# Performance work log

Measured on AMD Instinct MI355X. Metric: run time of the kernel, lower is better.

## Reference

```python
import jax, jax.numpy as jnp
import numpy as np


def setup_inputs() -> dict:
    key = jax.random.key(0)
    k1, k2, k3 = jax.random.split(key, 3)
    N = 20000
    # valid [x1, y1, x2, y2] boxes: centers in [0,1000), sizes in [1,101)
    xy = jax.random.uniform(k1, (N, 2), dtype=jnp.float32) * 1000.0
    wh = jax.random.uniform(k2, (N, 2), dtype=jnp.float32) * 100.0 + 1.0
    boxes = jnp.concatenate([xy, xy + wh], axis=1)
    scores = jax.random.uniform(k3, (N,), dtype=jnp.float32)
    return {
        "boxes": boxes,
        "scores": scores,
        "max_output_size": 1000,
        "iou_threshold": 0.5,
        "scores_threshold": 0.1,
    }


def reference(boxes, scores, max_output_size, iou_threshold, scores_threshold):
    boxes = boxes.astype(jnp.float32)
    scores = scores.astype(jnp.float32)
    N = boxes.shape[0]

    # score filtering: instead of physically filtering (dynamic shape),
    # mark below-threshold boxes as pre-suppressed and push them to the
    # end of the stable descending sort with -inf keys.
    valid = scores > scores_threshold
    sort_key = jnp.where(valid, scores, -jnp.inf)
    order = jnp.argsort(-sort_key)  # jnp.argsort is stable -> stable descending

    sboxes = boxes[order]                      # [N,4] score-sorted boxes
    svalid = valid[order]
    sorig = order.astype(jnp.int32)            # original indices, sorted
    areas = (sboxes[:, 2] - sboxes[:, 0]) * (sboxes[:, 3] - sboxes[:, 1])
    idx = jnp.arange(N)

    def body(carry, i):
        suppressed, selected, count = carry
        can = jnp.logical_and(~suppressed[i], count < max_output_size)
        selected = jnp.where(can, selected.at[count].set(sorig[i]), selected)
        # vectorized IoU of box i against all boxes (only j > i matter)
        b = sboxes[i]
        x1 = jnp.maximum(b[0], sboxes[:, 0])
        y1 = jnp.maximum(b[1], sboxes[:, 1])
        x2 = jnp.minimum(b[2], sboxes[:, 2])
        y2 = jnp.minimum(b[3], sboxes[:, 3])
        inter = jnp.maximum(x2 - x1, 0.0) * jnp.maximum(y2 - y1, 0.0)
        union = jnp.maximum(areas[i] + areas - inter, 1e-6)
        iou = inter / union
        suppressed = suppressed | (can & (idx > i) & (iou >= iou_threshold))
        count = count + can.astype(jnp.int32)
        return (suppressed, selected, count), None

    init = (~svalid, jnp.zeros(max_output_size, dtype=jnp.int32), jnp.int32(0))
    (_, selected, count), _ = jax.lax.scan(body, init, idx)
    return selected, count
```

## Files before the change

kernel.cpp:

```cpp
#include <hip/hip_runtime.h>
#include <cstdint>

typedef unsigned long long u64;

#define TOPK 2048
#define MW2 (TOPK / 64)
#define CAND 4096
#define HIST_BLOCKS 8
#define COMPACT_BLOCKS 32
#define FB_WORDS 1024


__device__ __forceinline__ unsigned score_ud(float s, float thr) {
    unsigned u = __float_as_uint(s);
    u ^= (u >> 31) ? 0xFFFFFFFFu : 0x80000000u;
    unsigned ud = ~u;
    if (!(s > thr)) ud = 0xFFFFFFFFu;
    return ud;
}

__global__ __launch_bounds__(256) void hist_kernel(const float* __restrict__ scores,
                                                   const float* __restrict__ thrPtr,
                                                   int* __restrict__ slices,
                                                   int* __restrict__ meta, int N) {
    __shared__ int h[4096];
    int tid = threadIdx.x;
    for (int b = tid; b < 4096; b += 256) h[b] = 0;
    if (blockIdx.x == 0 && tid == 0) meta[0] = 0;
    __syncthreads();
    float thr = *thrPtr;
    for (int i = blockIdx.x * 256 + tid; i < N; i += HIST_BLOCKS * 256) {
        unsigned ud = score_ud(scores[i], thr);
        if (ud != 0xFFFFFFFFu) atomicAdd(&h[ud >> 20], 1);
    }
    __syncthreads();
    int* myslice = slices + blockIdx.x * 4096;
    for (int b = tid; b < 4096; b += 256) myslice[b] = h[b];
}

__global__ __launch_bounds__(256) void compact_kernel(
        const float* __restrict__ scores, const float* __restrict__ thrPtr,
        const int* __restrict__ slices, int* __restrict__ meta,
        u64* __restrict__ ckeys, int N, int maxNeed) {
    __shared__ int bins[4096];
    __shared__ int shC;
    int tid = threadIdx.x, lane = tid & 63;
    {
        const int4* sl = (const int4*)slices;
        int4* bo = (int4*)bins;
#pragma unroll
        for (int k = 0; k < 4; ++k) {
            int p = k * 256 + tid;
            int4 a = sl[p];
            int4 v1 = sl[1024 + p];
            int4 v2 = sl[2 * 1024 + p];
            int4 v3 = sl[3 * 1024 + p];
            int4 v4 = sl[4 * 1024 + p];
            int4 v5 = sl[5 * 1024 + p];
            int4 v6 = sl[6 * 1024 + p];
            int4 v7 = sl[7 * 1024 + p];
            a.x += v1.x + v2.x + v3.x + v4.x + v5.x + v6.x + v7.x;
            a.y += v1.y + v2.y + v3.y + v4.y + v5.y + v6.y + v7.y;
            a.z += v1.z + v2.z + v3.z + v4.z + v5.z + v6.z + v7.z;
            a.w += v1.w + v2.w + v3.w + v4.w + v5.w + v6.w + v7.w;
            bo[p] = a;
        }
    }
    __syncthreads();
    if (tid < 64) {
        int base = lane * 64;
        int sum = 0;
        for (int b = 0; b < 64; ++b) sum += bins[base + ((b + lane) & 63)];
        int incl = sum;
        for (int off = 1; off < 64; off <<= 1) {
            int o = __shfl_up(incl, off, 64);
            if (lane >= off) incl += o;
        }
        int total = __shfl(incl, 63, 64);
        int need = (maxNeed < total) ? maxNeed : total;
        u64 ok = __ballot(incl >= need);
        int L = (ok != 0ull) ? (int)__builtin_ctzll(ok) : 0;
        if (lane == L) {
            int acc = incl - sum;
            int C = base, Msel = acc;
            for (int b = 0; b < 64; ++b) {
                acc += bins[base + b];
                if (acc >= need) { C = base + b; Msel = acc; break; }
            }
            if (need <= 0) { C = -1; Msel = 0; }
            shC = C;
            if (blockIdx.x == 0) {
                meta[2] = Msel;
                meta[3] = (Msel > CAND) ? 1 : 0;
            }
        }
        if (lane == 0 && blockIdx.x == 0) meta[1] = total;
    }
    __syncthreads();
    int C = shC;
    float thr = *thrPtr;
    for (int i0 = blockIdx.x * 256; i0 < N; i0 += COMPACT_BLOCKS * 256) {
        int i = i0 + tid;
        bool sel = false;
        unsigned ud = 0;
        if (i < N) {
            ud = score_ud(scores[i], thr);
            sel = (ud != 0xFFFFFFFFu) && ((int)(ud >> 20) <= C);
        }
        u64 ball = __ballot(sel);
        if (ball) {
            int cntw = __popcll(ball);
            int base = 0;
            if (lane == 0) base = atomicAdd(&meta[0], cntw);
            base = __shfl(base, 0, 64);
            if (sel) {
                int slot = base + __popcll(ball & ((1ull << lane) - 1ull));
                if (slot < CAND) ckeys[slot] = ((u64)ud << 32) | (unsigned)i;
            }
        }
    }
}

template<int K>
__device__ __forceinline__ void wave_chain(u64 (&r)[4], int wave, int lane) {
    if (K >= 256) {
#pragma unroll
        for (int e = 0; e < 2; ++e) {
            bool up = ((((wave << 8) | (e << 6) | lane) & K) == 0);
            if ((r[e] > r[e + 2]) == up) { u64 tmp = r[e]; r[e] = r[e + 2]; r[e + 2] = tmp; }
        }
    }
    if (K >= 128) {
#pragma unroll
        for (int e = 0; e < 4; e += 2) {
            bool up = ((((wave << 8) | (e << 6) | lane) & K) == 0);
            if ((r[e] > r[e + 1]) == up) { u64 tmp = r[e]; r[e] = r[e + 1]; r[e + 1] = tmp; }
        }
    }
#pragma unroll
    for (int j = 32; j >= 1; j >>= 1) {
        if (2 * j <= K) {
#pragma unroll
            for (int e = 0; e < 4; ++e) {
                bool up = ((((wave << 8) | (e << 6) | lane) & K) == 0);
                u64 o = __shfl_xor(r[e], j, 64);
                bool lower = ((lane & j) == 0);
                bool keepMin = (up == lower);
                u64 mn = (r[e] < o) ? r[e] : o;
                u64 mx = (r[e] < o) ? o : r[e];
                r[e] = keepMin ? mn : mx;
            }
        }
    }
}

__global__ __launch_bounds__(1024) void sort_gather_kernel(
        const u64* __restrict__ ckeys, const int* __restrict__ meta,
        const float* __restrict__ boxes,
        float* __restrict__ sx1, float* __restrict__ sy1,
        float* __restrict__ sx2, float* __restrict__ sy2,
        float* __restrict__ areas, int* __restrict__ sorig,
        u64* __restrict__ validw) {
    __shared__ u64 lk[CAND];
    int tid = threadIdx.x, lane = tid & 63, wave = tid >> 6;
    int M = meta[2];
    if (M > CAND) M = CAND;
    u64 r[4];
#pragma unroll
    for (int e = 0; e < 4; ++e) {
        int s = (wave << 8) + (e << 6) + lane;
        r[e] = (s < M) ? ckeys[s] : ~0ull;
    }
    wave_chain<2>(r, wave, lane);
    wave_chain<4>(r, wave, lane);
    wave_chain<8>(r, wave, lane);
    wave_chain<16>(r, wave, lane);
    wave_chain<32>(r, wave, lane);
    wave_chain<64>(r, wave, lane);
    wave_chain<128>(r, wave, lane);
    wave_chain<256>(r, wave, lane);
#pragma unroll
    for (int lvl = 0; lvl < 4; ++lvl) {
        const int K = 512 << lvl;
#pragma unroll
        for (int e = 0; e < 4; ++e) lk[(wave << 8) + (e << 6) + lane] = r[e];
        __syncthreads();
        for (int j = K / 2; j >= 256; j >>= 1) {
            for (int p = tid; p < CAND / 2; p += 1024) {
                int i = ((p & ~(j - 1)) << 1) | (p & (j - 1));
                int l = i + j;
                bool up = ((i & K) == 0);
                u64 a = lk[i], b = lk[l];
                if ((a > b) == up) { lk[i] = b; lk[l] = a; }
            }
            __syncthreads();
        }
#pragma unroll
        for (int e = 0; e < 4; ++e) r[e] = lk[(wave << 8) + (e << 6) + lane];
        switch (lvl) {
            case 0: wave_chain<512>(r, wave, lane); break;
            case 1: wave_chain<1024>(r, wave, lane); break;
            case 2: wave_chain<2048>(r, wave, lane); break;
            default: wave_chain<4096>(r, wave, lane); break;
        }
    }
    if (wave < (TOPK / 256)) {
#pragma unroll
        for (int e = 0; e < 4; ++e) {
            int s = (wave << 8) + (e << 6) + lane;
            u64 k = r[e];
            unsigned hi = (unsigned)(k >> 32), lo = (unsigned)k;
            bool valid = (hi != 0xFFFFFFFFu);
            u64 ball = __ballot(valid);
            if (lane == 0) validw[s >> 6] = ball;
            float4 b; b.x = 0.f; b.y = 0.f; b.z = 0.f; b.w = 0.f;
            if (valid) b = ((const float4*)boxes)[lo];
            sx1[s] = b.x; sy1[s] = b.y; sx2[s] = b.z; sy2[s] = b.w;
            areas[s] = (b.z - b.x) * (b.w - b.y);
            sorig[s] = valid ? (int)lo : 0;
        }
    }
}

__global__ __launch_bounds__(64) void mask2_kernel(
        const float* __restrict__ sx1, const float* __restrict__ sy1,
        const float* __restrict__ sx2, const float* __restrict__ sy2,
        const float* __restrict__ areas, const float* __restrict__ iouThrPtr,
        u64* __restrict__ maskT, u64* __restrict__ diagT) {
    int wi = blockIdx.x, wj = blockIdx.y;
    if (wj < wi) return;
    __shared__ float jx1[64], jy1[64], jx2[64], jy2[64], ja[64];
    __shared__ u64 rowLDS[64];
    int t = threadIdx.x;
    int j0 = wj << 6;
    jx1[t] = sx1[j0 + t]; jy1[t] = sy1[j0 + t];
    jx2[t] = sx2[j0 + t]; jy2[t] = sy2[j0 + t];
    ja[t] = areas[j0 + t];
    __syncthreads();
    int i = (wi << 6) + t;
    float thr = *iouThrPtr;
    float ix1 = sx1[i], iy1 = sy1[i], ix2 = sx2[i], iy2 = sy2[i], ia = areas[i];
    u64 bits = 0;
    for (int jj = 0; jj < 64; ++jj) {
        int j = j0 + jj;
        if (j > i) {
            float xx1 = fmaxf(ix1, jx1[jj]);
            float yy1 = fmaxf(iy1, jy1[jj]);
            float xx2 = fminf(ix2, jx2[jj]);
            float yy2 = fminf(iy2, jy2[jj]);
            float ww = fmaxf(xx2 - xx1, 0.0f);
            float hh = fmaxf(yy2 - yy1, 0.0f);
            float inter = ww * hh;
            float uni = fmaxf(ia + ja[jj] - inter, 1e-6f);
            if (inter / uni >= thr) bits |= 1ull << jj;
        }
    }
    rowLDS[t] = bits;
    __syncthreads();
    u64 col = 0;
    for (int r = 0; r < 64; ++r) col |= ((rowLDS[r] >> t) & 1ull) << r;
    maskT[(size_t)(j0 + t) * MW2 + wi] = col;
    if (wi == wj) diagT[(wi << 6) + t] = col;
}

__global__ __launch_bounds__(1024) void scan2_kernel(
        const u64* __restrict__ maskT, const u64* __restrict__ diagT,
        const u64* __restrict__ validw, const int* __restrict__ sorig,
        const int* __restrict__ meta,
        const float* __restrict__ boxes, const float* __restrict__ scores,
        const float* __restrict__ iouThrPtr, const float* __restrict__ scoreThrPtr,
        int* __restrict__ out, int N, int maxOut) {
    __shared__ u64 diagLDS[TOPK];
    __shared__ u64 selw[MW2];
    __shared__ u64 validwLDS[MW2];
    __shared__ u64 ballots[4];
    __shared__ int selLDS[TOPK];
    __shared__ int cntSh;
    __shared__ int validScanSh;
    __shared__ u64 aliveW[FB_WORDS];
    __shared__ u64 keyRed[16];
    __shared__ u64 winKeySh;
    int tid = threadIdx.x, lane = tid & 63, wave = tid >> 6;

    for (int k = tid; k < TOPK; k += 1024) diagLDS[k] = diagT[k];
    if (tid < MW2) { selw[tid] = 0ull; validwLDS[tid] = validw[tid]; }
    if (tid == 0) { cntSh = 0; validScanSh = 0; }

    ulonglong2 a0, a1, a2, a3;
    int cc = tid >> 2, g = tid & 3;
    if (tid < 256) {
        const ulonglong2* p = (const ulonglong2*)(maskT + (size_t)cc * MW2 + g * 8);
        a0 = p[0]; a1 = p[1]; a2 = p[2]; a3 = p[3];
    }
    __syncthreads();

    int cnt = 0;
    for (int w = 0; w < MW2; ++w) {
        if (tid < 256) {
            u64 wd0 = a0.x, wd1 = a0.y, wd2 = a1.x, wd3 = a1.y;
            u64 wd4 = a2.x, wd5 = a2.y, wd6 = a3.x, wd7 = a3.y;
            int wr0 = g * 8;
            u64 acc = 0;
            if (wr0 + 0 < w) acc |= wd0 & selw[wr0 + 0];
            if (wr0 + 1 < w) acc |= wd1 & selw[wr0 + 1];
            if (wr0 + 2 < w) acc |= wd2 & selw[wr0 + 2];
            if (wr0 + 3 < w) acc |= wd3 & selw[wr0 + 3];
            if (wr0 + 4 < w) acc |= wd4 & selw[wr0 + 4];
            if (wr0 + 5 < w) acc |= wd5 & selw[wr0 + 5];
            if (wr0 + 6 < w) acc |= wd6 & selw[wr0 + 6];
            if (wr0 + 7 < w) acc |= wd7 & selw[wr0 + 7];
            acc |= __shfl_xor(acc, 1, 64);
            acc |= __shfl_xor(acc, 2, 64);
            u64 B = __ballot(acc != 0ull);
            if (lane == 0) ballots[wave] = B;
            if (w + 1 < MW2) {
                const ulonglong2* p = (const ulonglong2*)(maskT + (size_t)((w + 1) * 64 + cc) * MW2 + g * 8);
                a0 = p[0]; a1 = p[1]; a2 = p[2]; a3 = p[3];
            }
        }
        __syncthreads();
        if (wave == 0) {
            u64 bv = ballots[lane >> 4];
            bool crossk = (bv >> ((lane & 15) << 2)) & 1ull;
            bool alv = ((validwLDS[w] >> lane) & 1ull) && !crossk;
            u64 inm = diagLDS[(w << 6) | lane];
            u64 sel = __ballot(alv);
            for (int it = 0; it < 64; ++it) {
                bool killed = (inm & sel) != 0ull;
                u64 ns = __ballot(alv && !killed);
                if (ns == sel) break;
                sel = ns;
            }
            int room = maxOut - cnt;
            int tot = __popcll(sel);
            u64 below = (1ull << lane) - 1ull;
            if (tot > room) {
                bool keep = ((sel >> lane) & 1ull) && (__popcll(sel & below) < room);
                sel = __ballot(keep);
                tot = room;
            }
            if ((sel >> lane) & 1ull) {
                int pos = cnt + __popcll(sel & below);
                selLDS[pos] = (w << 6) | lane;
            }
            if (lane == 0) { selw[w] = sel; cntSh = cnt + tot; }
        }
        __syncthreads();
        cnt = cntSh;
        if (cnt >= maxOut) break;
    }

    if (tid < MW2) atomicAdd(&validScanSh, __popcll(validwLDS[tid]));
    __syncthreads();
    int vt = meta[1];
    int f2 = meta[3];
    bool complete = (f2 == 0) && ((cnt >= maxOut) || (validScanSh >= vt));
    if (complete) {
        for (int k = tid; k < cnt; k += 1024) out[k] = sorig[selLDS[k]];
        for (int k = cnt + tid; k < maxOut; k += 1024) out[k] = 0;
        if (tid == 0) out[maxOut] = cnt;
        return;
    }

    float sThr = *scoreThrPtr, iThr = *iouThrPtr;
    for (int e0 = wave << 6; e0 < N; e0 += 1024) {
        int e = e0 + lane;
        bool a = (e < N) && (scores[e] > sThr);
        u64 ball = __ballot(a);
        if (lane == 0) aliveW[e0 >> 6] = ball;
    }
    __syncthreads();
    int fcnt = 0;
    while (fcnt < maxOut) {
        u64 best = 0;
        for (int e = tid; e < N; e += 1024) {
            if ((aliveW[e >> 6] >> (e & 63)) & 1ull) {
                float s = scores[e];
                unsigned u = __float_as_uint(s);
                u ^= (u >> 31) ? 0xFFFFFFFFu : 0x80000000u;
                u64 k = ((u64)u << 32) | (unsigned)(~e);
                if (k > best) best = k;
            }
        }
#pragma unroll
        for (int off = 32; off >= 1; off >>= 1) {
            u64 o = __shfl_xor(best, off, 64);
            if (o > best) best = o;
        }
        if (lane == 0) keyRed[wave] = best;
        __syncthreads();
        if (tid == 0) {
            u64 b = 0;
            for (int p = 0; p < 16; ++p) if (keyRed[p] > b) b = keyRed[p];
            winKeySh = b;
        }
        __syncthreads();
        u64 wk = winKeySh;
        if (wk == 0ull) break;
        int win = (int)(~(unsigned)wk);
        if (tid == 0) out[fcnt] = win;
        ++fcnt;
        float4 wb = ((const float4*)boxes)[win];
        float wa = (wb.z - wb.x) * (wb.w - wb.y);
        for (int e0 = wave << 6; e0 < N; e0 += 1024) {
            int e = e0 + lane;
            bool kill = false;
            if (e < N && ((aliveW[e0 >> 6] >> lane) & 1ull)) {
                if (e == win) kill = true;
                else {
                    float4 bb = ((const float4*)boxes)[e];
                    float xx1 = fmaxf(wb.x, bb.x), yy1 = fmaxf(wb.y, bb.y);
                    float xx2 = fminf(wb.z, bb.z), yy2 = fminf(wb.w, bb.w);
                    float inter = fmaxf(xx2 - xx1, 0.0f) * fmaxf(yy2 - yy1, 0.0f);
                    float ba = (bb.z - bb.x) * (bb.w - bb.y);
                    float uni = fmaxf(wa + ba - inter, 1e-6f);
                    kill = (inter / uni >= iThr);
                }
            }
            u64 kb = __ballot(kill);
            if (lane == 0 && kb) aliveW[e0 >> 6] &= ~kb;
        }
        __syncthreads();
    }
    for (int k = fcnt + tid; k < maxOut; k += 1024) out[k] = 0;
    if (tid == 0) out[maxOut] = fcnt;
}

extern "C" void kernel_launch(void* const* d_in, const int* in_sizes, int n_in,
                              void* d_out, int out_size, void* d_ws, size_t ws_size,
                              hipStream_t stream) {
    const float* boxes       = (const float*)d_in[0];
    const float* scores      = (const float*)d_in[1];
    const float* iouThrPtr   = (const float*)d_in[3];
    const float* scoreThrPtr = (const float*)d_in[4];

    int N = in_sizes[0] / 4;
    int maxOut = out_size - 1;

    char* ws = (char*)d_ws;
    size_t off = 0;
    auto take = [&](size_t b) { void* p = ws + off; off = (off + b + 255) & ~(size_t)255; return p; };
    int*   slices = (int*)  take((size_t)HIST_BLOCKS * 4096 * 4);
    int*   meta   = (int*)  take(256);
    u64*   ckeys  = (u64*)  take((size_t)CAND * 8);
    float* sx1    = (float*)take(TOPK * 4);
    float* sy1    = (float*)take(TOPK * 4);
    float* sx2    = (float*)take(TOPK * 4);
    float* sy2    = (float*)take(TOPK * 4);
    float* areas  = (float*)take(TOPK * 4);
    int*   sorig  = (int*)  take(TOPK * 4);
    u64*   validw = (u64*)  take(MW2 * 8);
    u64*   maskT  = (u64*)  take((size_t)TOPK * MW2 * 8);
    u64*   diagT  = (u64*)  take((size_t)MW2 * 64 * 8);
    (void)ws_size;

    hist_kernel<<<HIST_BLOCKS, 256, 0, stream>>>(scores, scoreThrPtr, slices, meta, N);
    compact_kernel<<<COMPACT_BLOCKS, 256, 0, stream>>>(scores, scoreThrPtr, slices, meta,
                                                       ckeys, N, TOPK);
    sort_gather_kernel<<<1, 1024, 0, stream>>>(ckeys, meta, boxes, sx1, sy1, sx2, sy2,
                                               areas, sorig, validw);
    mask2_kernel<<<dim3(MW2, MW2), 64, 0, stream>>>(sx1, sy1, sx2, sy2, areas, iouThrPtr,
                                                    maskT, diagT);
    scan2_kernel<<<1, 1024, 0, stream>>>(maskT, diagT, validw, sorig, meta,
                                         boxes, scores, iouThrPtr, scoreThrPtr,
                                         (int*)d_out, N, maxOut);
}
```

Baseline: 76.75 us.

## Fuse histogram, compaction and sort into a single-block select kernel

Merges the multi-block histogram, compaction and bitonic sort kernels into one 1024-thread block that builds the score histogram in shared memory, compacts candidates directly into shared memory, and sorts them in place. This removes two kernel launches and the global round-trips through slices and ckeys, plus global atomics. In exchange, the scan over 20000 scores runs twice on a single CU instead of being spread across many blocks.

```diff
diff --git a/kernel.cpp b/kernel.cpp
--- a/kernel.cpp
+++ b/kernel.cpp
@@ -6,8 +6,6 @@
 #define TOPK 2048
 #define MW2 (TOPK / 64)
 #define CAND 4096
-#define HIST_BLOCKS 8
-#define COMPACT_BLOCKS 32
 #define FB_WORDS 1024
 
 
@@ -19,51 +17,63 @@
     return ud;
 }
 
-__global__ __launch_bounds__(256) void hist_kernel(const float* __restrict__ scores,
-                                                   const float* __restrict__ thrPtr,
-                                                   int* __restrict__ slices,
-                                                   int* __restrict__ meta, int N) {
-    __shared__ int h[4096];
-    int tid = threadIdx.x;
-    for (int b = tid; b < 4096; b += 256) h[b] = 0;
-    if (blockIdx.x == 0 && tid == 0) meta[0] = 0;
-    __syncthreads();
+template<int K>
+__device__ __forceinline__ void wave_chain(u64 (&r)[4], int wave, int lane) {
+    if (K >= 256) {
+#pragma unroll
+        for (int e = 0; e < 2; ++e) {
+            bool up = ((((wave << 8) | (e << 6) | lane) & K) == 0);
+            if ((r[e] > r[e + 2]) == up) { u64 tmp = r[e]; r[e] = r[e + 2]; r[e + 2] = tmp; }
+        }
+    }
+    if (K >= 128) {
+#pragma unroll
+        for (int e = 0; e < 4; e += 2) {
+            bool up = ((((wave << 8) | (e << 6) | lane) & K) == 0);
+            if ((r[e] > r[e + 1]) == up) { u64 tmp = r[e]; r[e] = r[e + 1]; r[e + 1] = tmp; }
+        }
+    }
+#pragma unroll
+    for (int j = 32; j >= 1; j >>= 1) {
+        if (2 * j <= K) {
+#pragma unroll
+            for (int e = 0; e < 4; ++e) {
+                bool up = ((((wave << 8) | (e << 6) | lane) & K) == 0);
+                u64 o = __shfl_xor(r[e], j, 64);
+                bool lower = ((lane & j) == 0);
+                bool keepMin = (up == lower);
+                u64 mn = (r[e] < o) ? r[e] : o;
+                u64 mx = (r[e] < o) ? o : r[e];
+                r[e] = keepMin ? mn : mx;
+            }
+        }
+    }
+}
+
+__global__ __launch_bounds__(1024) void fused_select_kernel(
+        const float* __restrict__ scores, const float* __restrict__ thrPtr,
+        const float* __restrict__ boxes, int* __restrict__ meta,
+        float* __restrict__ sx1, float* __restrict__ sy1,
+        float* __restrict__ sx2, float* __restrict__ sy2,
+        float* __restrict__ areas, int* __restrict__ sorig,
+        u64* __restrict__ validw, int N, int maxNeed) {
+    __shared__ int bins[4096];
+    __shared__ u64 lk[CAND];
+    __shared__ int shC;
+    __shared__ int shTicket;
+    int tid = threadIdx.x, lane = tid & 63, wave = tid >> 6;
+
+    for (int b = tid; b < 4096; b += 1024) bins[b] = 0;
+    for (int u = tid; u < CAND; u += 1024) lk[u] = ~0ull;
+    if (tid == 0) shTicket = 0;
+    __syncthreads();
+
     float thr = *thrPtr;
-    for (int i = blockIdx.x * 256 + tid; i < N; i += HIST_BLOCKS * 256) {
-        unsigned ud = score_ud(scores[i], thr);
-        if (ud != 0xFFFFFFFFu) atomicAdd(&h[ud >> 20], 1);
-    }
-    __syncthreads();
-    int* myslice = slices + blockIdx.x * 4096;
-    for (int b = tid; b < 4096; b += 256) myslice[b] = h[b];
-}
-
-__global__ __launch_bounds__(256) void compact_kernel(
-        const float* __restrict__ scores, const float* __restrict__ thrPtr,
-        const int* __restrict__ slices, int* __restrict__ meta,
-        u64* __restrict__ ckeys, int N, int maxNeed) {
-    __shared__ int bins[4096];
-    __shared__ int shC;
-    int tid = threadIdx.x, lane = tid & 63;
-    {
-        const int4* sl = (const int4*)slices;
-        int4* bo = (int4*)bins;
-#pragma unroll
-        for (int k = 0; k < 4; ++k) {
-            int p = k * 256 + tid;
-            int4 a = sl[p];
-            int4 v1 = sl[1024 + p];
-            int4 v2 = sl[2 * 1024 + p];
-            int4 v3 = sl[3 * 1024 + p];
-            int4 v4 = sl[4 * 1024 + p];
-            int4 v5 = sl[5 * 1024 + p];
-            int4 v6 = sl[6 * 1024 + p];
-            int4 v7 = sl[7 * 1024 + p];
-            a.x += v1.x + v2.x + v3.x + v4.x + v5.x + v6.x + v7.x;
-            a.y += v1.y + v2.y + v3.y + v4.y + v5.y + v6.y + v7.y;
-            a.z += v1.z + v2.z + v3.z + v4.z + v5.z + v6.z + v7.z;
-            a.w += v1.w + v2.w + v3.w + v4.w + v5.w + v6.w + v7.w;
-            bo[p] = a;
+    for (int i0 = 0; i0 < N; i0 += 1024) {
+        int i = i0 + tid;
+        if (i < N) {
+            unsigned ud = score_ud(scores[i], thr);
+            if (ud != 0xFFFFFFFFu) atomicAdd(&bins[ud >> 20], 1);
         }
     }
     __syncthreads();
@@ -89,17 +99,14 @@
             }
             if (need <= 0) { C = -1; Msel = 0; }
             shC = C;
-            if (blockIdx.x == 0) {
-                meta[2] = Msel;
-                meta[3] = (Msel > CAND) ? 1 : 0;
-            }
-        }
-        if (lane == 0 && blockIdx.x == 0) meta[1] = total;
+            meta[2] = Msel;
+            meta[3] = (Msel > CAND) ? 1 : 0;
+        }
+        if (lane == 0) meta[1] = total;
     }
     __syncthreads();
     int C = shC;
-    float thr = *thrPtr;
-    for (int i0 = blockIdx.x * 256; i0 < N; i0 += COMPACT_BLOCKS * 256) {
+    for (int i0 = 0; i0 < N; i0 += 1024) {
         int i = i0 + tid;
         bool sel = false;
         unsigned ud = 0;
@@ -111,66 +118,18 @@
         if (ball) {
             int cntw = __popcll(ball);
             int base = 0;
-            if (lane == 0) base = atomicAdd(&meta[0], cntw);
+            if (lane == 0) base = atomicAdd(&shTicket, cntw);
             base = __shfl(base, 0, 64);
             if (sel) {
                 int slot = base + __popcll(ball & ((1ull << lane) - 1ull));
-                if (slot < CAND) ckeys[slot] = ((u64)ud << 32) | (unsigned)i;
-            }
-        }
-    }
-}
-
-template<int K>
-__device__ __forceinline__ void wave_chain(u64 (&r)[4], int wave, int lane) {
-    if (K >= 256) {
-#pragma unroll
-        for (int e = 0; e < 2; ++e) {
-            bool up = ((((wave << 8) | (e << 6) | lane) & K) == 0);
-            if ((r[e] > r[e + 2]) == up) { u64 tmp = r[e]; r[e] = r[e + 2]; r[e + 2] = tmp; }
-        }
-    }
-    if (K >= 128) {
-#pragma unroll
-        for (int e = 0; e < 4; e += 2) {
-            bool up = ((((wave << 8) | (e << 6) | lane) & K) == 0);
-            if ((r[e] > r[e + 1]) == up) { u64 tmp = r[e]; r[e] = r[e + 1]; r[e + 1] = tmp; }
-        }
-    }
-#pragma unroll
-    for (int j = 32; j >= 1; j >>= 1) {
-        if (2 * j <= K) {
-#pragma unroll
-            for (int e = 0; e < 4; ++e) {
-                bool up = ((((wave << 8) | (e << 6) | lane) & K) == 0);
-                u64 o = __shfl_xor(r[e], j, 64);
-                bool lower = ((lane & j) == 0);
-                bool keepMin = (up == lower);
-                u64 mn = (r[e] < o) ? r[e] : o;
-                u64 mx = (r[e] < o) ? o : r[e];
-                r[e] = keepMin ? mn : mx;
-            }
-        }
-    }
-}
-
-__global__ __launch_bounds__(1024) void sort_gather_kernel(
-        const u64* __restrict__ ckeys, const int* __restrict__ meta,
-        const float* __restrict__ boxes,
-        float* __restrict__ sx1, float* __restrict__ sy1,
-        float* __restrict__ sx2, float* __restrict__ sy2,
-        float* __restrict__ areas, int* __restrict__ sorig,
-        u64* __restrict__ validw) {
-    __shared__ u64 lk[CAND];
-    int tid = threadIdx.x, lane = tid & 63, wave = tid >> 6;
-    int M = meta[2];
-    if (M > CAND) M = CAND;
+                if (slot < CAND) lk[slot] = ((u64)ud << 32) | (unsigned)i;
+            }
+        }
+    }
+    __syncthreads();
     u64 r[4];
 #pragma unroll
-    for (int e = 0; e < 4; ++e) {
-        int s = (wave << 8) + (e << 6) + lane;
-        r[e] = (s < M) ? ckeys[s] : ~0ull;
-    }
+    for (int e = 0; e < 4; ++e) r[e] = lk[(wave << 8) + (e << 6) + lane];
     wave_chain<2>(r, wave, lane);
     wave_chain<4>(r, wave, lane);
     wave_chain<8>(r, wave, lane);
@@ -440,9 +399,7 @@
     char* ws = (char*)d_ws;
     size_t off = 0;
     auto take = [&](size_t b) { void* p = ws + off; off = (off + b + 255) & ~(size_t)255; return p; };
-    int*   slices = (int*)  take((size_t)HIST_BLOCKS * 4096 * 4);
     int*   meta   = (int*)  take(256);
-    u64*   ckeys  = (u64*)  take((size_t)CAND * 8);
     float* sx1    = (float*)take(TOPK * 4);
     float* sy1    = (float*)take(TOPK * 4);
     float* sx2    = (float*)take(TOPK * 4);
@@ -454,11 +411,9 @@
     u64*   diagT  = (u64*)  take((size_t)MW2 * 64 * 8);
     (void)ws_size;
 
-    hist_kernel<<<HIST_BLOCKS, 256, 0, stream>>>(scores, scoreThrPtr, slices, meta, N);
-    compact_kernel<<<COMPACT_BLOCKS, 256, 0, stream>>>(scores, scoreThrPtr, slices, meta,
-                                                       ckeys, N, TOPK);
-    sort_gather_kernel<<<1, 1024, 0, stream>>>(ckeys, meta, boxes, sx1, sy1, sx2, sy2,
-                                               areas, sorig, validw);
+    fused_select_kernel<<<1, 1024, 0, stream>>>(scores, scoreThrPtr, boxes, meta,
+                                                sx1, sy1, sx2, sy2, areas, sorig,
+                                                validw, N, TOPK);
     mask2_kernel<<<dim3(MW2, MW2), 64, 0, stream>>>(sx1, sy1, sx2, sy2, areas, iouThrPtr,
                                                     maskT, diagT);
     scan2_kernel<<<1, 1024, 0, stream>>>(maskT, diagT, validw, sorig, meta,
```

Result: faster. 75.21 us (-2.0%).

## Run greedy NMS block scan in a single wave with double-buffered mask columns

Applied to the files above, without the earlier changes.

The serial 64-box block scan now runs entirely in wave 0. Each lane loads its full 32-word suppression column into registers and double-buffers the next column, which removes the two block-wide barriers per step and the cross-wave ballot exchange. The histogram stage also doubles its block count, and the compaction sums the slices in a loop. The trade-off is higher register pressure, since 64 ulonglong2 values are held per lane, and all cross-block AND work now falls on one wave instead of four.

```diff
diff --git a/kernel.cpp b/kernel.cpp
--- a/kernel.cpp
+++ b/kernel.cpp
@@ -6,7 +6,7 @@
 #define TOPK 2048
 #define MW2 (TOPK / 64)
 #define CAND 4096
-#define HIST_BLOCKS 8
+#define HIST_BLOCKS 16
 #define COMPACT_BLOCKS 32
 #define FB_WORDS 1024
 
@@ -51,19 +51,14 @@
 #pragma unroll
         for (int k = 0; k < 4; ++k) {
             int p = k * 256 + tid;
-            int4 a = sl[p];
-            int4 v1 = sl[1024 + p];
-            int4 v2 = sl[2 * 1024 + p];
-            int4 v3 = sl[3 * 1024 + p];
-            int4 v4 = sl[4 * 1024 + p];
-            int4 v5 = sl[5 * 1024 + p];
-            int4 v6 = sl[6 * 1024 + p];
-            int4 v7 = sl[7 * 1024 + p];
-            a.x += v1.x + v2.x + v3.x + v4.x + v5.x + v6.x + v7.x;
-            a.y += v1.y + v2.y + v3.y + v4.y + v5.y + v6.y + v7.y;
-            a.z += v1.z + v2.z + v3.z + v4.z + v5.z + v6.z + v7.z;
-            a.w += v1.w + v2.w + v3.w + v4.w + v5.w + v6.w + v7.w;
-            bo[p] = a;
+            int ax = 0, ay = 0, az = 0, aw = 0;
+#pragma unroll
+            for (int s = 0; s < HIST_BLOCKS; ++s) {
+                int4 v = sl[s * 1024 + p];
+                ax += v.x; ay += v.y; az += v.z; aw += v.w;
+            }
+            int4 o; o.x = ax; o.y = ay; o.z = az; o.w = aw;
+            bo[p] = o;
         }
     }
     __syncthreads();
@@ -273,7 +268,6 @@
     __shared__ u64 diagLDS[TOPK];
     __shared__ u64 selw[MW2];
     __shared__ u64 validwLDS[MW2];
-    __shared__ u64 ballots[4];
     __shared__ int selLDS[TOPK];
     __shared__ int cntSh;
     __shared__ int validScanSh;
@@ -285,73 +279,68 @@
     for (int k = tid; k < TOPK; k += 1024) diagLDS[k] = diagT[k];
     if (tid < MW2) { selw[tid] = 0ull; validwLDS[tid] = validw[tid]; }
     if (tid == 0) { cntSh = 0; validScanSh = 0; }
-
-    ulonglong2 a0, a1, a2, a3;
-    int cc = tid >> 2, g = tid & 3;
-    if (tid < 256) {
-        const ulonglong2* p = (const ulonglong2*)(maskT + (size_t)cc * MW2 + g * 8);
-        a0 = p[0]; a1 = p[1]; a2 = p[2]; a3 = p[3];
-    }
-    __syncthreads();
-
-    int cnt = 0;
-    for (int w = 0; w < MW2; ++w) {
-        if (tid < 256) {
-            u64 wd0 = a0.x, wd1 = a0.y, wd2 = a1.x, wd3 = a1.y;
-            u64 wd4 = a2.x, wd5 = a2.y, wd6 = a3.x, wd7 = a3.y;
-            int wr0 = g * 8;
-            u64 acc = 0;
-            if (wr0 + 0 < w) acc |= wd0 & selw[wr0 + 0];
-            if (wr0 + 1 < w) acc |= wd1 & selw[wr0 + 1];
-            if (wr0 + 2 < w) acc |= wd2 & selw[wr0 + 2];
-            if (wr0 + 3 < w) acc |= wd3 & selw[wr0 + 3];
-            if (wr0 + 4 < w) acc |= wd4 & selw[wr0 + 4];
-            if (wr0 + 5 < w) acc |= wd5 & selw[wr0 + 5];
-            if (wr0 + 6 < w) acc |= wd6 & selw[wr0 + 6];
-            if (wr0 + 7 < w) acc |= wd7 & selw[wr0 + 7];
-            acc |= __shfl_xor(acc, 1, 64);
-            acc |= __shfl_xor(acc, 2, 64);
-            u64 B = __ballot(acc != 0ull);
-            if (lane == 0) ballots[wave] = B;
-            if (w + 1 < MW2) {
-                const ulonglong2* p = (const ulonglong2*)(maskT + (size_t)((w + 1) * 64 + cc) * MW2 + g * 8);
-                a0 = p[0]; a1 = p[1]; a2 = p[2]; a3 = p[3];
-            }
-        }
-        __syncthreads();
-        if (wave == 0) {
-            u64 bv = ballots[lane >> 4];
-            bool crossk = (bv >> ((lane & 15) << 2)) & 1ull;
-            bool alv = ((validwLDS[w] >> lane) & 1ull) && !crossk;
-            u64 inm = diagLDS[(w << 6) | lane];
-            u64 sel = __ballot(alv);
-            for (int it = 0; it < 64; ++it) {
-                bool killed = (inm & sel) != 0ull;
-                u64 ns = __ballot(alv && !killed);
-                if (ns == sel) break;
-                sel = ns;
-            }
-            int room = maxOut - cnt;
-            int tot = __popcll(sel);
-            u64 below = (1ull << lane) - 1ull;
-            if (tot > room) {
-                bool keep = ((sel >> lane) & 1ull) && (__popcll(sel & below) < room);
-                sel = __ballot(keep);
-                tot = room;
-            }
-            if ((sel >> lane) & 1ull) {
-                int pos = cnt + __popcll(sel & below);
-                selLDS[pos] = (w << 6) | lane;
-            }
-            if (lane == 0) { selw[w] = sel; cntSh = cnt + tot; }
-        }
-        __syncthreads();
-        cnt = cntSh;
-        if (cnt >= maxOut) break;
-    }
+    __syncthreads();
+
+    if (wave == 0) {
+        ulonglong2 A[16], B[16];
+#define LOADCOL(BUF, W)                                                          \
+        {                                                                        \
+            const ulonglong2* p =                                                \
+                (const ulonglong2*)(maskT + (size_t)(((W) << 6) | lane) * MW2);  \
+            _Pragma("unroll")                                                    \
+            for (int k = 0; k < 16; ++k) BUF[k] = p[k];                          \
+        }
+#define PROCESS(BUF, W)                                                          \
+        {                                                                        \
+            u64 kill = 0;                                                        \
+            _Pragma("unroll")                                                    \
+            for (int k = 0; k < 16; ++k)                                         \
+                kill |= (BUF[k].x & selw[2 * k]) | (BUF[k].y & selw[2 * k + 1]); \
+            bool alv = ((validwLDS[W] >> lane) & 1ull) && (kill == 0ull);        \
+            u64 inm = diagLDS[((W) << 6) | lane];                                \
+            u64 sel = __ballot(alv);                                             \
+            for (int it = 0; it < 64; ++it) {                                    \
+                bool killed = (inm & sel) != 0ull;                               \
+                u64 ns = __ballot(alv && !killed);                               \
+                if (ns == sel) break;                                            \
+                sel = ns;                                                        \
+            }                                                                    \
+            int room = maxOut - cnt;                                             \
+            int tot = __popcll(sel);                                             \
+            u64 below = (1ull << lane) - 1ull;                                   \
+            if (tot > room) {                                                    \
+                bool keep = ((sel >> lane) & 1ull) &&                            \
+                            (__popcll(sel & below) < room);                      \
+                sel = __ballot(keep);                                            \
+                tot = room;                                                      \
+            }                                                                    \
+            if ((sel >> lane) & 1ull) {                                          \
+                int pos = cnt + __popcll(sel & below);                           \
+                selLDS[pos] = ((W) << 6) | lane;                                 \
+            }                                                                    \
+            if (lane == 0) selw[W] = sel;                                        \
+            cnt += tot;                                                          \
+            done = (cnt >= maxOut);                                              \
+        }
+        int cnt = 0;
+        bool done = false;
+        LOADCOL(A, 0);
+        for (int w = 0; w < MW2 && !done; w += 2) {
+            if (w + 1 < MW2) LOADCOL(B, w + 1);
+            PROCESS(A, w);
+            if (done || w + 1 >= MW2) break;
+            if (w + 2 < MW2) LOADCOL(A, w + 2);
+            PROCESS(B, w + 1);
+        }
+#undef LOADCOL
+#undef PROCESS
+        if (lane == 0) cntSh = cnt;
+    }
+    __syncthreads();
 
     if (tid < MW2) atomicAdd(&validScanSh, __popcll(validwLDS[tid]));
     __syncthreads();
+    int cnt = cntSh;
     int vt = meta[1];
     int f2 = meta[3];
     bool complete = (f2 == 0) && ((cnt >= maxOut) || (validScanSh >= vt));
```

New measurement: 93.06 us. 1.21x slower.

## Replace single-block bitonic sort with multi-block rank-by-counting gather

Applied to the files above, without the earlier changes.

The 4096-element bitonic sort, which ran in one 1024-thread block, is replaced by a rank kernel launched over 64 blocks. Each block loads all candidate keys into LDS and computes each key's rank by counting smaller keys, then scatters the box and original index directly to that rank. Boxes are now stored as float4, and mask2 recomputes areas on the fly. The valid-word bitmask is derived from the candidate count instead of being stored. This trades O(M^2) comparisons and redundant LDS loads per block for parallelism across many CUs instead of one, and it relies on keys being unique, which the embedded index guarantees.

```diff
diff --git a/kernel.cpp b/kernel.cpp
--- a/kernel.cpp
+++ b/kernel.cpp
@@ -8,6 +8,7 @@
 #define CAND 4096
 #define HIST_BLOCKS 8
 #define COMPACT_BLOCKS 32
+#define RANK_BLOCKS (CAND / 64)
 #define FB_WORDS 1024
 
 
@@ -121,111 +122,40 @@
     }
 }
 
-template<int K>
-__device__ __forceinline__ void wave_chain(u64 (&r)[4], int wave, int lane) {
-    if (K >= 256) {
-#pragma unroll
-        for (int e = 0; e < 2; ++e) {
-            bool up = ((((wave << 8) | (e << 6) | lane) & K) == 0);
-            if ((r[e] > r[e + 2]) == up) { u64 tmp = r[e]; r[e] = r[e + 2]; r[e + 2] = tmp; }
-        }
-    }
-    if (K >= 128) {
-#pragma unroll
-        for (int e = 0; e < 4; e += 2) {
-            bool up = ((((wave << 8) | (e << 6) | lane) & K) == 0);
-            if ((r[e] > r[e + 1]) == up) { u64 tmp = r[e]; r[e] = r[e + 1]; r[e + 1] = tmp; }
-        }
-    }
-#pragma unroll
-    for (int j = 32; j >= 1; j >>= 1) {
-        if (2 * j <= K) {
-#pragma unroll
-            for (int e = 0; e < 4; ++e) {
-                bool up = ((((wave << 8) | (e << 6) | lane) & K) == 0);
-                u64 o = __shfl_xor(r[e], j, 64);
-                bool lower = ((lane & j) == 0);
-                bool keepMin = (up == lower);
-                u64 mn = (r[e] < o) ? r[e] : o;
-                u64 mx = (r[e] < o) ? o : r[e];
-                r[e] = keepMin ? mn : mx;
-            }
-        }
-    }
-}
-
-__global__ __launch_bounds__(1024) void sort_gather_kernel(
+__global__ __launch_bounds__(256) void rank_gather_kernel(
         const u64* __restrict__ ckeys, const int* __restrict__ meta,
         const float* __restrict__ boxes,
-        float* __restrict__ sx1, float* __restrict__ sy1,
-        float* __restrict__ sx2, float* __restrict__ sy2,
-        float* __restrict__ areas, int* __restrict__ sorig,
-        u64* __restrict__ validw) {
+        float4* __restrict__ sboxes, int* __restrict__ sorig) {
     __shared__ u64 lk[CAND];
-    int tid = threadIdx.x, lane = tid & 63, wave = tid >> 6;
-    int M = meta[2];
-    if (M > CAND) M = CAND;
-    u64 r[4];
-#pragma unroll
-    for (int e = 0; e < 4; ++e) {
-        int s = (wave << 8) + (e << 6) + lane;
-        r[e] = (s < M) ? ckeys[s] : ~0ull;
-    }
-    wave_chain<2>(r, wave, lane);
-    wave_chain<4>(r, wave, lane);
-    wave_chain<8>(r, wave, lane);
-    wave_chain<16>(r, wave, lane);
-    wave_chain<32>(r, wave, lane);
-    wave_chain<64>(r, wave, lane);
-    wave_chain<128>(r, wave, lane);
-    wave_chain<256>(r, wave, lane);
-#pragma unroll
-    for (int lvl = 0; lvl < 4; ++lvl) {
-        const int K = 512 << lvl;
-#pragma unroll
-        for (int e = 0; e < 4; ++e) lk[(wave << 8) + (e << 6) + lane] = r[e];
-        __syncthreads();
-        for (int j = K / 2; j >= 256; j >>= 1) {
-            for (int p = tid; p < CAND / 2; p += 1024) {
-                int i = ((p & ~(j - 1)) << 1) | (p & (j - 1));
-                int l = i + j;
-                bool up = ((i & K) == 0);
-                u64 a = lk[i], b = lk[l];
-                if ((a > b) == up) { lk[i] = b; lk[l] = a; }
-            }
-            __syncthreads();
-        }
-#pragma unroll
-        for (int e = 0; e < 4; ++e) r[e] = lk[(wave << 8) + (e << 6) + lane];
-        switch (lvl) {
-            case 0: wave_chain<512>(r, wave, lane); break;
-            case 1: wave_chain<1024>(r, wave, lane); break;
-            case 2: wave_chain<2048>(r, wave, lane); break;
-            default: wave_chain<4096>(r, wave, lane); break;
-        }
-    }
-    if (wave < (TOPK / 256)) {
-#pragma unroll
-        for (int e = 0; e < 4; ++e) {
-            int s = (wave << 8) + (e << 6) + lane;
-            u64 k = r[e];
-            unsigned hi = (unsigned)(k >> 32), lo = (unsigned)k;
-            bool valid = (hi != 0xFFFFFFFFu);
-            u64 ball = __ballot(valid);
-            if (lane == 0) validw[s >> 6] = ball;
-            float4 b; b.x = 0.f; b.y = 0.f; b.z = 0.f; b.w = 0.f;
-            if (valid) b = ((const float4*)boxes)[lo];
-            sx1[s] = b.x; sy1[s] = b.y; sx2[s] = b.z; sy2[s] = b.w;
-            areas[s] = (b.z - b.x) * (b.w - b.y);
-            sorig[s] = valid ? (int)lo : 0;
+    __shared__ int part[4][64];
+    int tid = threadIdx.x, lane = tid & 63, q = tid >> 6;
+    int Msel = meta[2];
+    if (Msel > CAND) Msel = CAND;
+    for (int j = tid; j < Msel; j += 256) lk[j] = ckeys[j];
+    __syncthreads();
+    if (blockIdx.x * 64 >= Msel) return;
+    int i = blockIdx.x * 64 + lane;
+    u64 key = (i < Msel) ? lk[i] : ~0ull;
+    int chunk = (Msel + 3) >> 2;
+    int j0 = q * chunk;
+    int j1 = j0 + chunk; if (j1 > Msel) j1 = Msel;
+    int r = 0;
+#pragma unroll 4
+    for (int j = j0; j < j1; ++j) r += (lk[j] < key) ? 1 : 0;
+    part[q][lane] = r;
+    __syncthreads();
+    if (q == 0 && i < Msel) {
+        int rank = part[0][lane] + part[1][lane] + part[2][lane] + part[3][lane];
+        if (rank < TOPK) {
+            int idx = (int)(key & 0xFFFFFFFFu);
+            sboxes[rank] = ((const float4*)boxes)[idx];
+            sorig[rank] = idx;
         }
     }
 }
 
 __global__ __launch_bounds__(64) void mask2_kernel(
-        const float* __restrict__ sx1, const float* __restrict__ sy1,
-        const float* __restrict__ sx2, const float* __restrict__ sy2,
-        const float* __restrict__ areas, const float* __restrict__ iouThrPtr,
+        const float4* __restrict__ sboxes, const float* __restrict__ iouThrPtr,
         u64* __restrict__ maskT, u64* __restrict__ diagT) {
     int wi = blockIdx.x, wj = blockIdx.y;
     if (wj < wi) return;
@@ -233,21 +163,22 @@
     __shared__ u64 rowLDS[64];
     int t = threadIdx.x;
     int j0 = wj << 6;
-    jx1[t] = sx1[j0 + t]; jy1[t] = sy1[j0 + t];
-    jx2[t] = sx2[j0 + t]; jy2[t] = sy2[j0 + t];
-    ja[t] = areas[j0 + t];
+    float4 jb = sboxes[j0 + t];
+    jx1[t] = jb.x; jy1[t] = jb.y; jx2[t] = jb.z; jy2[t] = jb.w;
+    ja[t] = (jb.z - jb.x) * (jb.w - jb.y);
     __syncthreads();
     int i = (wi << 6) + t;
     float thr = *iouThrPtr;
-    float ix1 = sx1[i], iy1 = sy1[i], ix2 = sx2[i], iy2 = sy2[i], ia = areas[i];
+    float4 ib = sboxes[i];
+    float ia = (ib.z - ib.x) * (ib.w - ib.y);
     u64 bits = 0;
     for (int jj = 0; jj < 64; ++jj) {
         int j = j0 + jj;
         if (j > i) {
-            float xx1 = fmaxf(ix1, jx1[jj]);
-            float yy1 = fmaxf(iy1, jy1[jj]);
-            float xx2 = fminf(ix2, jx2[jj]);
-            float yy2 = fminf(iy2, jy2[jj]);
+            float xx1 = fmaxf(ib.x, jx1[jj]);
+            float yy1 = fmaxf(ib.y, jy1[jj]);
+            float xx2 = fminf(ib.z, jx2[jj]);
+            float yy2 = fminf(ib.w, jy2[jj]);
             float ww = fmaxf(xx2 - xx1, 0.0f);
             float hh = fmaxf(yy2 - yy1, 0.0f);
             float inter = ww * hh;
@@ -265,8 +196,7 @@
 
 __global__ __launch_bounds__(1024) void scan2_kernel(
         const u64* __restrict__ maskT, const u64* __restrict__ diagT,
-        const u64* __restrict__ validw, const int* __restrict__ sorig,
-        const int* __restrict__ meta,
+        const int* __restrict__ sorig, const int* __restrict__ meta,
         const float* __restrict__ boxes, const float* __restrict__ scores,
         const float* __restrict__ iouThrPtr, const float* __restrict__ scoreThrPtr,
         int* __restrict__ out, int N, int maxOut) {
@@ -276,15 +206,21 @@
     __shared__ u64 ballots[4];
     __shared__ int selLDS[TOPK];
     __shared__ int cntSh;
-    __shared__ int validScanSh;
     __shared__ u64 aliveW[FB_WORDS];
     __shared__ u64 keyRed[16];
     __shared__ u64 winKeySh;
     int tid = threadIdx.x, lane = tid & 63, wave = tid >> 6;
 
+    int Msel = meta[2];
+    int V = (Msel < TOPK) ? Msel : TOPK;
     for (int k = tid; k < TOPK; k += 1024) diagLDS[k] = diagT[k];
-    if (tid < MW2) { selw[tid] = 0ull; validwLDS[tid] = validw[tid]; }
-    if (tid == 0) { cntSh = 0; validScanSh = 0; }
+    if (tid < MW2) {
+        int lo = tid * 64;
+        u64 vw = (V >= lo + 64) ? ~0ull : ((V > lo) ? ((1ull << (V - lo)) - 1ull) : 0ull);
+        validwLDS[tid] = vw;
+        selw[tid] = 0ull;
+    }
+    if (tid == 0) cntSh = 0;
 
     ulonglong2 a0, a1, a2, a3;
     int cc = tid >> 2, g = tid & 3;
@@ -350,11 +286,9 @@
         if (cnt >= maxOut) break;
     }
 
-    if (tid < MW2) atomicAdd(&validScanSh, __popcll(validwLDS[tid]));
-    __syncthreads();
     int vt = meta[1];
     int f2 = meta[3];
-    bool complete = (f2 == 0) && ((cnt >= maxOut) || (validScanSh >= vt));
+    bool complete = (f2 == 0) && ((cnt >= maxOut) || (V >= vt));
     if (complete) {
         for (int k = tid; k < cnt; k += 1024) out[k] = sorig[selLDS[k]];
         for (int k = cnt + tid; k < maxOut; k += 1024) out[k] = 0;
@@ -440,28 +374,21 @@
     char* ws = (char*)d_ws;
     size_t off = 0;
     auto take = [&](size_t b) { void* p = ws + off; off = (off + b + 255) & ~(size_t)255; return p; };
-    int*   slices = (int*)  take((size_t)HIST_BLOCKS * 4096 * 4);
-    int*   meta   = (int*)  take(256);
-    u64*   ckeys  = (u64*)  take((size_t)CAND * 8);
-    float* sx1    = (float*)take(TOPK * 4);
-    float* sy1    = (float*)take(TOPK * 4);
-    float* sx2    = (float*)take(TOPK * 4);
-    float* sy2    = (float*)take(TOPK * 4);
-    float* areas  = (float*)take(TOPK * 4);
-    int*   sorig  = (int*)  take(TOPK * 4);
-    u64*   validw = (u64*)  take(MW2 * 8);
-    u64*   maskT  = (u64*)  take((size_t)TOPK * MW2 * 8);
-    u64*   diagT  = (u64*)  take((size_t)MW2 * 64 * 8);
+    int*    slices = (int*)   take((size_t)HIST_BLOCKS * 4096 * 4);
+    int*    meta   = (int*)   take(256);
+    u64*    ckeys  = (u64*)   take((size_t)CAND * 8);
+    float4* sboxes = (float4*)take((size_t)TOPK * 16);
+    int*    sorig  = (int*)   take((size_t)TOPK * 4);
+    u64*    maskT  = (u64*)   take((size_t)TOPK * MW2 * 8);
+    u64*    diagT  = (u64*)   take((size_t)MW2 * 64 * 8);
     (void)ws_size;
 
     hist_kernel<<<HIST_BLOCKS, 256, 0, stream>>>(scores, scoreThrPtr, slices, meta, N);
     compact_kernel<<<COMPACT_BLOCKS, 256, 0, stream>>>(scores, scoreThrPtr, slices, meta,
                                                        ckeys, N, TOPK);
-    sort_gather_kernel<<<1, 1024, 0, stream>>>(ckeys, meta, boxes, sx1, sy1, sx2, sy2,
-                                               areas, sorig, validw);
-    mask2_kernel<<<dim3(MW2, MW2), 64, 0, stream>>>(sx1, sy1, sx2, sy2, areas, iouThrPtr,
-                                                    maskT, diagT);
-    scan2_kernel<<<1, 1024, 0, stream>>>(maskT, diagT, validw, sorig, meta,
+    rank_gather_kernel<<<RANK_BLOCKS, 256, 0, stream>>>(ckeys, meta, boxes, sboxes, sorig);
+    mask2_kernel<<<dim3(MW2, MW2), 64, 0, stream>>>(sboxes, iouThrPtr, maskT, diagT);
+    scan2_kernel<<<1, 1024, 0, stream>>>(maskT, diagT, sorig, meta,
                                          boxes, scores, iouThrPtr, scoreThrPtr,
                                          (int*)d_out, N, maxOut);
 }
```

Measured after the change: 64.54 us. 15.9% less time.
